# Kernel optimization log

Measured on AMD Instinct MI355X. Metric: run time of the kernel, lower is better.

## Reference

```python
import jax, jax.numpy as jnp
import numpy as np

# Model constants (from init_kwargs)
B, S, D = 2, 2048, 2048          # batch, seq, d_model
E = 64                           # num_routed_experts
TOP_K = 4
BOT = int(D * 0.25)              # bottle_dim = 512
EXP = 1536                       # routed expert hidden (bigmac_expert_size)
DFF = 8192                       # shared expert hidden (d_ff)
Z_LOSS_W = 1e-4
MOE_SCALE = 0.5                  # 1/(1 + [num_shared_experts>0])


def setup_inputs() -> dict:
    key = jax.random.key(0)
    ks = jax.random.split(key, 10)
    std = 0.011
    return {
        "x": jax.random.normal(ks[0], (B, S, D), jnp.float32),
        "router_w": jax.random.normal(ks[1], (E, D), jnp.float32) * 0.02,
        "gate_w": jax.random.normal(ks[2], (DFF, D), jnp.float32) * std,
        "up_w": jax.random.normal(ks[3], (DFF, D), jnp.float32) * std,
        "down_w": jax.random.normal(ks[4], (D, DFF), jnp.float32) * std,
        "w_down": jax.random.normal(ks[5], (BOT, D), jnp.float32) * std,
        "w_up": jax.random.normal(ks[6], (D, BOT), jnp.float32) * std,
        "w12": jax.random.normal(ks[7], (E, BOT, 2 * EXP), jnp.float32) * std,
        "w3": jax.random.normal(ks[8], (E, EXP, BOT), jnp.float32) * std,
    }


def reference(x, router_w, gate_w, up_w, down_w, w_down, w_up, w12, w3):
    b, s, d = x.shape
    h = x.reshape(-1, d)                       # [N, D]
    N = h.shape[0]
    NT = N * TOP_K                             # total routed token-slots

    # ---- router (fp32) ----
    logits = h @ router_w.T                    # [N, E]
    scores = jax.nn.sigmoid(logits)
    z_loss = jnp.mean(jnp.nan_to_num(logits) ** 2) * Z_LOSS_W
    # expert_bias is None -> selection_scores == scores
    _, topk_idx = jax.lax.top_k(scores, TOP_K)             # [N, K]
    topk_logits = jnp.take_along_axis(logits, topk_idx, axis=1)
    gating = jax.nn.softmax(topk_logits, axis=-1)          # [N, K]

    # ---- shared expert (SwiGLU) ----
    shared = (jax.nn.silu(h @ gate_w.T) * (h @ up_w.T)) @ down_w.T  # [N, D]

    # ---- bottleneck down-projection ----
    down = h @ w_down.T                        # [N, BOT]

    # ---- dispatch: sort tokens by expert, capacity-limited padding ----
    flat = topk_idx.reshape(-1)                # [NT]
    order = jnp.argsort(flat)                  # stable sort
    sorted_e = flat[order]
    counts = jax.ops.segment_sum(jnp.ones(NT, jnp.int32), flat, num_segments=E)
    ptr = jnp.cumsum(counts) - counts          # expert start offsets
    local = jnp.arange(NT) - ptr[sorted_e]     # rank within expert
    max_load = (NT // E // 8 + 6) * 8          # capacity per expert
    num_slots = E * max_load
    mask = local < max_load
    slots = sorted_e * max_load + local
    token_idx = jnp.repeat(jnp.arange(N), TOP_K)

    # reverse_map[slot] = source token row (N = dummy row); extra slot absorbs dropped tokens
    rev = jnp.full(num_slots + 1, N, dtype=jnp.int32)
    rev = rev.at[jnp.where(mask, slots, num_slots)].set(token_idx[order].astype(jnp.int32))
    rev = rev[:num_slots]

    h_dummy = jnp.concatenate([down, jnp.zeros((1, BOT), down.dtype)], axis=0)
    padding = h_dummy[rev].reshape(E, max_load, BOT)

    # ---- grouped expert GEMMs ----
    h12 = jnp.einsum('eld,edf->elf', padding, w12)   # [E, max_load, 2*EXP]
    h1, h2 = jnp.split(h12, 2, axis=-1)
    po = jnp.einsum('elf,efd->eld', jax.nn.silu(h1) * h2, w3)  # [E, max_load, BOT]
    po = jnp.concatenate([po.reshape(-1, BOT), jnp.zeros((1, BOT), po.dtype)], axis=0)

    # ---- combine: gather back, weight by gating ----
    gm = jnp.full(NT, num_slots, dtype=jnp.int32)
    gm = gm.at[order].set(jnp.where(mask, slots, num_slots).astype(jnp.int32))
    gathered = po[gm].reshape(N, TOP_K, BOT)
    routed = jnp.einsum('nk,nkd->nd', gating, gathered) @ w_up.T  # [N, D]

    # eval mode: route_scale = 1.0, aux_loss = 0
    out = ((shared + routed) * MOE_SCALE).reshape(b, s, d)
    return out, z_loss
```

## Files before the change

kernel.cpp:

```cpp
#include <hip/hip_runtime.h>

#define DEV __device__ __forceinline__

typedef __attribute__((ext_vector_type(4))) float f4;
typedef __attribute__((ext_vector_type(8))) __bf16 bfrag;
typedef __attribute__((ext_vector_type(4))) unsigned short us4;
typedef __attribute__((ext_vector_type(8))) unsigned short us8;

#define NTOK   4096
#define DMODEL 2048
#define NEXP   64
#define MAXLD  304
#define NSLOT  19456

DEV unsigned short f2bf(float f){
  union { float f; unsigned int i; } u; u.f = f;
  unsigned int r = u.i + 0x7fffu + ((u.i >> 16) & 1u);
  return (unsigned short)(r >> 16);
}
DEV float bf2f(unsigned short b){
  union { unsigned int i; float f; } u; u.i = ((unsigned int)b) << 16;
  return u.f;
}
DEV float silu_f(float g){ return g / (1.0f + __expf(-g)); }

DEV void gl_lds16(const unsigned short* g, unsigned short* l){
  __builtin_amdgcn_global_load_lds(
      (const __attribute__((address_space(1))) void*)g,
      (__attribute__((address_space(3))) void*)l, 16, 0, 0);
}

template<int BM, int EPI>
__global__ __launch_bounds__(512, 1) void gemm2(
    const unsigned short* __restrict__ A, const unsigned short* __restrict__ B,
    void* __restrict__ Cp, const float* __restrict__ addin, int M, int N, int K,
    void* __restrict__ Cp2, void* __restrict__ Cp3)
{
  constexpr int ALD = BM / 128;
  constexpr int MQ  = BM / 64;
  constexpr int HR  = BM / 2;
  __shared__ unsigned short As[2][2][HR * 64];
  __shared__ unsigned short Bs[2][2][128 * 64];

  const int nwg = gridDim.x * gridDim.y;
  int bid = blockIdx.y * gridDim.x + blockIdx.x;
  bid = (bid & 7) * (nwg >> 3) + (bid >> 3);
  const int bx = bid % gridDim.x, by = bid / gridDim.x;
  const int bm = by * BM, bn = bx * 256;

  const int t = threadIdx.x, lane = t & 63, wave = t >> 6;
  const int ha = wave >> 2;
  const int wn = (wave & 3) * 64;
  const int hb = wn >> 7;
  const int cb = wn & 127;
  const int fr = lane & 15, kg = lane >> 4;

  const int r0 = t >> 3;
  const int s0 = (t & 7) ^ (r0 & 7);

#define STG_AH(d_, h_, s_) do {                                                          \
    gl_lds16(A + (long long)(bm + (h_) * HR + r0) * K + (long long)(s_) * 64 + s0 * 8,   \
             &As[d_][h_][(wave * 64) * 8]);                                              \
    if (ALD == 2)                                                                        \
      gl_lds16(A + (long long)(bm + (h_) * HR + r0 + 64) * K + (long long)(s_) * 64 + s0 * 8, \
               &As[d_][h_][(512 + wave * 64) * 8]);                                      \
  } while (0)
#define STG_BH(d_, h_, s_) do {                                                          \
    gl_lds16(B + (long long)(bn + (h_) * 128 + r0) * K + (long long)(s_) * 64 + s0 * 8,  \
             &Bs[d_][h_][(wave * 64) * 8]);                                              \
    gl_lds16(B + (long long)(bn + (h_) * 128 + r0 + 64) * K + (long long)(s_) * 64 + s0 * 8, \
             &Bs[d_][h_][(512 + wave * 64) * 8]);                                        \
  } while (0)

  f4 acc[2 * MQ][4];
#pragma unroll
  for (int m = 0; m < 2 * MQ; ++m)
#pragma unroll
    for (int n = 0; n < 4; ++n) acc[m][n] = f4{0.f, 0.f, 0.f, 0.f};

  const int ns = K >> 6;

  STG_BH(0, 0, 0); STG_AH(0, 0, 0); STG_BH(0, 1, 0); STG_AH(0, 1, 0);
  STG_BH(1, 0, 1); STG_AH(1, 0, 1);
  asm volatile("s_waitcnt vmcnt(%0)" :: "i"(2 + ALD) : "memory");
  __builtin_amdgcn_s_barrier();

  for (int tt = 0; tt < ns; ++tt){
    const int d = tt & 1, nd = d ^ 1;
    bfrag af[MQ][2], bf[2][2][2];

#pragma unroll
    for (int ni = 0; ni < 2; ++ni)
#pragma unroll
      for (int kh = 0; kh < 2; ++kh){
        const int cn = cb + ni * 16 + fr;
        bf[0][ni][kh] = *(const bfrag*)&Bs[d][hb][cn * 64 + ((((kh << 2) | kg) ^ (cn & 7)) << 3)];
      }
#pragma unroll
    for (int mi = 0; mi < MQ; ++mi)
#pragma unroll
      for (int kh = 0; kh < 2; ++kh){
        const int rh = mi * 16 + fr;
        af[mi][kh] = *(const bfrag*)&As[d][ha][rh * 64 + ((((kh << 2) | kg) ^ (rh & 7)) << 3)];
      }
    if (tt + 1 < ns) STG_BH(nd, 1, tt + 1);
    if constexpr (BM == 256) asm volatile("s_waitcnt lgkmcnt(8)");
    else                     asm volatile("s_waitcnt lgkmcnt(4)");
    __builtin_amdgcn_s_barrier();
    asm volatile("s_waitcnt lgkmcnt(0)");
    __builtin_amdgcn_s_setprio(1);
#pragma unroll
    for (int mi = 0; mi < MQ; ++mi)
#pragma unroll
      for (int ni = 0; ni < 2; ++ni)
#pragma unroll
        for (int kh = 0; kh < 2; ++kh)
          acc[mi][ni] = __builtin_amdgcn_mfma_f32_16x16x32_bf16(af[mi][kh], bf[0][ni][kh], acc[mi][ni], 0, 0, 0);
    __builtin_amdgcn_s_setprio(0);
    __builtin_amdgcn_s_barrier();

#pragma unroll
    for (int ni = 0; ni < 2; ++ni)
#pragma unroll
      for (int kh = 0; kh < 2; ++kh){
        const int cn = cb + 32 + ni * 16 + fr;
        bf[1][ni][kh] = *(const bfrag*)&Bs[d][hb][cn * 64 + ((((kh << 2) | kg) ^ (cn & 7)) << 3)];
      }
    if (tt + 1 < ns) STG_AH(nd, 1, tt + 1);
    __builtin_amdgcn_s_barrier();
    asm volatile("s_waitcnt lgkmcnt(0)");
    __builtin_amdgcn_s_setprio(1);
#pragma unroll
    for (int mi = 0; mi < MQ; ++mi)
#pragma unroll
      for (int ni = 0; ni < 2; ++ni)
#pragma unroll
        for (int kh = 0; kh < 2; ++kh)
          acc[mi][2 + ni] = __builtin_amdgcn_mfma_f32_16x16x32_bf16(af[mi][kh], bf[1][ni][kh], acc[mi][2 + ni], 0, 0, 0);
    __builtin_amdgcn_s_setprio(0);
    __builtin_amdgcn_s_barrier();

#pragma unroll
    for (int mi = 0; mi < MQ; ++mi)
#pragma unroll
      for (int kh = 0; kh < 2; ++kh){
        const int rh = MQ * 16 + mi * 16 + fr;
        af[mi][kh] = *(const bfrag*)&As[d][ha][rh * 64 + ((((kh << 2) | kg) ^ (rh & 7)) << 3)];
      }
    if (tt + 2 < ns) STG_BH(d, 0, tt + 2);
    __builtin_amdgcn_s_barrier();
    asm volatile("s_waitcnt lgkmcnt(0)");
    __builtin_amdgcn_s_setprio(1);
#pragma unroll
    for (int mi = 0; mi < MQ; ++mi)
#pragma unroll
      for (int ni = 0; ni < 2; ++ni)
#pragma unroll
        for (int kh = 0; kh < 2; ++kh)
          acc[MQ + mi][2 + ni] = __builtin_amdgcn_mfma_f32_16x16x32_bf16(af[mi][kh], bf[1][ni][kh], acc[MQ + mi][2 + ni], 0, 0, 0);
    __builtin_amdgcn_s_setprio(0);
    __builtin_amdgcn_s_barrier();

    if (tt + 2 < ns) STG_AH(d, 0, tt + 2);
    __builtin_amdgcn_s_barrier();
    __builtin_amdgcn_s_setprio(1);
#pragma unroll
    for (int mi = 0; mi < MQ; ++mi)
#pragma unroll
      for (int ni = 0; ni < 2; ++ni)
#pragma unroll
        for (int kh = 0; kh < 2; ++kh)
          acc[MQ + mi][ni] = __builtin_amdgcn_mfma_f32_16x16x32_bf16(af[mi][kh], bf[0][ni][kh], acc[MQ + mi][ni], 0, 0, 0);
    __builtin_amdgcn_s_setprio(0);
    if (tt + 2 < ns)      asm volatile("s_waitcnt vmcnt(%0)" :: "i"(2 + ALD) : "memory");
    else if (tt + 1 < ns) asm volatile("s_waitcnt vmcnt(0)" ::: "memory");
    if (tt + 1 < ns) __builtin_amdgcn_s_barrier();
  }

  if constexpr (EPI == 3){
    const int base = bn + wn;
    if (base < 16384){
      const int colb = base >> 1;
#pragma unroll
      for (int mh = 0; mh < 2; ++mh)
#pragma unroll
        for (int mi = 0; mi < MQ; ++mi){
          const int row0 = bm + ha * HR + mh * (HR / 2) + mi * 16 + kg * 4;
#pragma unroll
          for (int p = 0; p < 2; ++p){
            f4 g = acc[mh * MQ + mi][2 * p];
            f4 u = acc[mh * MQ + mi][2 * p + 1];
#pragma unroll
            for (int r = 0; r < 4; ++r)
              ((unsigned short*)Cp)[(long long)(row0 + r) * 8192 + colb + p * 16 + fr]
                = f2bf(silu_f(g[r]) * u[r]);
          }
        }
    } else if (base < 16896){
      const int cb2 = base - 16384;
#pragma unroll
      for (int mh = 0; mh < 2; ++mh)
#pragma unroll
        for (int mi = 0; mi < MQ; ++mi){
          const int row0 = bm + ha * HR + mh * (HR / 2) + mi * 16 + kg * 4;
#pragma unroll
          for (int nf = 0; nf < 4; ++nf){
            f4 v = acc[mh * MQ + mi][nf];
#pragma unroll
            for (int r = 0; r < 4; ++r)
              ((unsigned short*)Cp2)[(long long)(row0 + r) * 512 + cb2 + nf * 16 + fr] = f2bf(v[r]);
          }
        }
    } else {
      const int cb3 = base - 16896;
#pragma unroll
      for (int mh = 0; mh < 2; ++mh)
#pragma unroll
        for (int mi = 0; mi < MQ; ++mi){
          const int row0 = bm + ha * HR + mh * (HR / 2) + mi * 16 + kg * 4;
#pragma unroll
          for (int nf = 0; nf < 4; ++nf){
            const int col = cb3 + nf * 16 + fr;
            f4 v = acc[mh * MQ + mi][nf];
            if (col < 64){
#pragma unroll
              for (int r = 0; r < 4; ++r)
                ((float*)Cp3)[(long long)(row0 + r) * 64 + col] = v[r];
            }
          }
        }
    }
    return;
  }
#pragma unroll
  for (int mh = 0; mh < 2; ++mh)
#pragma unroll
    for (int mi = 0; mi < MQ; ++mi){
      const int row0 = bm + ha * HR + mh * (HR / 2) + mi * 16 + kg * 4;
#pragma unroll
      for (int nf = 0; nf < 4; ++nf){
        const int col = bn + wn + nf * 16 + fr;
        f4 v = acc[mh * MQ + mi][nf];
#pragma unroll
        for (int r = 0; r < 4; ++r){
          const long long off = (long long)(row0 + r) * N + col;
          if (EPI == 0)      ((unsigned short*)Cp)[off] = f2bf(v[r]);
          else if (EPI == 1) ((float*)Cp)[off] = v[r];
          else               ((float*)Cp)[off] = (v[r] + addin[off]) * 0.5f;
        }
      }
    }
#undef STG_AH
#undef STG_BH
}

template<int EPI>
__global__ __launch_bounds__(256) void gemm_bt(
    const unsigned short* __restrict__ A, const unsigned short* __restrict__ B,
    void* __restrict__ Cp, const float* __restrict__ addin,
    int M, int N, int K, long long sA, long long sB, long long sC)
{
  __shared__ unsigned short As[128*32];
  __shared__ unsigned short Bs[128*32];
  A += (long long)blockIdx.z * sA;
  B += (long long)blockIdx.z * sB;
  const long long cbase = (long long)blockIdx.z * sC;
  const int bm = blockIdx.y * 128, bn = blockIdx.x * 128;
  const int t = threadIdx.x, wave = t >> 6, lane = t & 63;
  const int wm = (wave >> 1) * 64, wn = (wave & 1) * 64;
  const int fr = lane & 15, kg = lane >> 4;

  f4 acc[4][4];
#pragma unroll
  for (int m = 0; m < 4; ++m)
#pragma unroll
    for (int n = 0; n < 4; ++n)
      acc[m][n] = f4{0.f, 0.f, 0.f, 0.f};

  const int i0 = t, i1 = 256 + t;
  int ar0 = bm + (i0 >> 2); if (ar0 > M - 1) ar0 = M - 1;
  int ar1 = bm + (i1 >> 2); if (ar1 > M - 1) ar1 = M - 1;
  int br0 = bn + (i0 >> 2); if (br0 > N - 1) br0 = N - 1;
  int br1 = bn + (i1 >> 2); if (br1 > N - 1) br1 = N - 1;
  const unsigned short* ap0 = A + (long long)ar0 * K + (i0 & 3) * 8;
  const unsigned short* ap1 = A + (long long)ar1 * K + (i1 & 3) * 8;
  const unsigned short* bp0 = B + (long long)br0 * K + (i0 & 3) * 8;
  const unsigned short* bp1 = B + (long long)br1 * K + (i1 & 3) * 8;
  unsigned short* da0 = As + wave * 512;
  unsigned short* da1 = As + 2048 + wave * 512;
  unsigned short* db0 = Bs + wave * 512;
  unsigned short* db1 = Bs + 2048 + wave * 512;

  for (int k0 = 0; k0 < K; k0 += 32){
    gl_lds16(ap0, da0);
    gl_lds16(ap1, da1);
    gl_lds16(bp0, db0);
    gl_lds16(bp1, db1);
    ap0 += 32; ap1 += 32; bp0 += 32; bp1 += 32;
    __syncthreads();
    bfrag af[4], bfv[4];
#pragma unroll
    for (int m = 0; m < 4; ++m) af[m] = *(const bfrag*)&As[(wm + m*16 + fr)*32 + kg*8];
#pragma unroll
    for (int n = 0; n < 4; ++n) bfv[n] = *(const bfrag*)&Bs[(wn + n*16 + fr)*32 + kg*8];
#pragma unroll
    for (int m = 0; m < 4; ++m)
#pragma unroll
      for (int n = 0; n < 4; ++n)
        acc[m][n] = __builtin_amdgcn_mfma_f32_16x16x32_bf16(af[m], bfv[n], acc[m][n], 0, 0, 0);
    __syncthreads();
  }

  if constexpr (EPI == 3){
    const int colb = (bn + wn) >> 1;
    const int ldo = N >> 1;
#pragma unroll
    for (int m = 0; m < 4; ++m){
      const int row0 = bm + wm + m*16 + kg*4;
#pragma unroll
      for (int p = 0; p < 2; ++p){
        f4 g = acc[m][2*p], u = acc[m][2*p+1];
#pragma unroll
        for (int r = 0; r < 4; ++r){
          const int row = row0 + r;
          if (row < M)
            ((unsigned short*)Cp)[cbase + (long long)row * ldo + colb + p*16 + fr]
              = f2bf(silu_f(g[r]) * u[r]);
        }
      }
    }
    return;
  }
#pragma unroll
  for (int m = 0; m < 4; ++m){
    const int row0 = bm + wm + m*16 + kg*4;
#pragma unroll
    for (int n = 0; n < 4; ++n){
      const int col = bn + wn + n*16 + fr;
      if (col < N){
        f4 v = acc[m][n];
#pragma unroll
        for (int r = 0; r < 4; ++r){
          const int row = row0 + r;
          if (row < M){
            const long long off = cbase + (long long)row * N + col;
            ((unsigned short*)Cp)[off] = f2bf(v[r]);
          }
        }
      }
    }
  }
}

__global__ void cvt_bf16(const float* __restrict__ in, unsigned short* __restrict__ out,
                         long long n4)
{
  long long i = (long long)blockIdx.x * 256 + threadIdx.x;
  if (i >= n4) return;
  float4 v = ((const float4*)in)[i];
  us4 o; o[0] = f2bf(v.x); o[1] = f2bf(v.y); o[2] = f2bf(v.z); o[3] = f2bf(v.w);
  ((us4*)out)[i] = o;
}

__global__ void cvt_rowmap(const float* __restrict__ in, unsigned short* __restrict__ out,
                           int hi)
{
  const long long idx = (long long)blockIdx.x * 256 + threadIdx.x;
  const int row = (int)(idx >> 9);
  const int c4 = ((int)idx & 511) << 2;
  const int orow = ((row >> 4) << 5) | (hi << 4) | (row & 15);
  float4 v = *(const float4*)(in + (long long)row * 2048 + c4);
  us4 o; o[0] = f2bf(v.x); o[1] = f2bf(v.y); o[2] = f2bf(v.z); o[3] = f2bf(v.w);
  *(us4*)(out + (long long)orow * 2048 + c4) = o;
}

template<int MODE>
__global__ __launch_bounds__(256) void transpose_cvt(const float* __restrict__ in,
    unsigned short* __restrict__ out, int R, int C)
{
  __shared__ float tile[32][33];
  const long long z = blockIdx.z;
  const float* ip = in + z * (long long)R * C;
  unsigned short* op = out + z * (long long)R * C;
  const int r0 = blockIdx.y * 32, c0 = blockIdx.x * 32;
  const int t = threadIdx.x;
  const int lr = t >> 3, lc = (t & 7) * 4;
  float4 v = *(const float4*)(ip + (long long)(r0 + lr) * C + c0 + lc);
  tile[lr][lc+0] = v.x; tile[lr][lc+1] = v.y; tile[lr][lc+2] = v.z; tile[lr][lc+3] = v.w;
  __syncthreads();
  const int oc = t >> 3, orr = (t & 7) * 4;
  us4 o;
  o[0] = f2bf(tile[orr+0][oc]); o[1] = f2bf(tile[orr+1][oc]);
  o[2] = f2bf(tile[orr+2][oc]); o[3] = f2bf(tile[orr+3][oc]);
  int c = c0 + oc;
  int orow;
  if (MODE == 1)
    orow = (c < 1536) ? (((c >> 4) << 5) | (c & 15))
                      : ((((c - 1536) >> 4) << 5) | 16 | ((c - 1536) & 15));
  else
    orow = c;
  *(us4*)(op + (long long)orow * R + r0 + orr) = o;
}

__global__ void router_topk(const float* __restrict__ logits, int* __restrict__ topk,
                            float* __restrict__ gating, float* __restrict__ zout)
{
  const int t = threadIdx.x, w = t >> 6, lane = t & 63;
  const int n = blockIdx.x * 4 + w;
  const float lg = logits[(long long)n * 64 + lane];
  float z = lg * lg;
#pragma unroll
  for (int off = 32; off; off >>= 1) z += __shfl_xor(z, off);
  __shared__ float zs[4];
  if (lane == 0) zs[w] = z;
  __syncthreads();
  if (t == 0) atomicAdd(zout, (zs[0]+zs[1]+zs[2]+zs[3]) * (0.0001f / 262144.0f));

  float cur = lg;
  float tl[4]; int ti[4];
#pragma unroll
  for (int k = 0; k < 4; ++k){
    float s = cur; int si = lane;
#pragma unroll
    for (int off = 32; off; off >>= 1){
      float so = __shfl_xor(s, off); int io = __shfl_xor(si, off);
      if (so > s || (so == s && io < si)){ s = so; si = io; }
    }
    tl[k] = s; ti[k] = si;
    if (lane == si) cur = -3.0e38f;
  }
  if (lane == 0){
    const float m0 = tl[0];
    const float e0 = __expf(tl[0]-m0), e1 = __expf(tl[1]-m0),
                e2 = __expf(tl[2]-m0), e3 = __expf(tl[3]-m0);
    const float inv = 1.0f / (e0 + e1 + e2 + e3);
    topk[n*4+0] = ti[0]; topk[n*4+1] = ti[1]; topk[n*4+2] = ti[2]; topk[n*4+3] = ti[3];
    gating[n*4+0] = e0*inv; gating[n*4+1] = e1*inv; gating[n*4+2] = e2*inv; gating[n*4+3] = e3*inv;
  }
}

__global__ void scan_route(const int* __restrict__ topk, int* __restrict__ gm,
                           int* __restrict__ rev, int* __restrict__ counts)
{
  const int e = blockIdx.x;
  const int t = threadIdx.x, w = t >> 6, lane = t & 63;
  __shared__ int wtot[4];
  int running = 0;
  for (int c = 0; c < 16384; c += 256){
    const int j = c + t;
    const bool p = (topk[j] == e);
    const unsigned long long m = __ballot(p);
    const int prefix = __popcll(m & ((1ull << lane) - 1ull));
    if (lane == 0) wtot[w] = __popcll(m);
    __syncthreads();
    int woff = 0;
#pragma unroll
    for (int i = 0; i < 4; ++i){ if (i < w) woff += wtot[i]; }
    const int btot = wtot[0] + wtot[1] + wtot[2] + wtot[3];
    if (p){
      const int rank = running + woff + prefix;
      gm[j] = (rank < MAXLD) ? (e * MAXLD + rank) : NSLOT;
      if (rank < MAXLD) rev[e * MAXLD + rank] = j >> 2;
    }
    running += btot;
    __syncthreads();
  }
  if (t == 0) counts[e] = running;
}

__global__ void gather_pad(const unsigned short* __restrict__ down, const int* __restrict__ rev,
                           const int* __restrict__ counts, unsigned short* __restrict__ pad)
{
  const int idx = blockIdx.x * 256 + threadIdx.x;
  const int s = idx >> 6, c8 = (idx & 63) * 8;
  const int e = s / MAXLD;
  const int r = s - e * MAXLD;
  int cnt = counts[e]; if (cnt > MAXLD) cnt = MAXLD;
  us8 v = {0,0,0,0,0,0,0,0};
  if (r < cnt){
    const int tok = rev[s];
    v = *(const us8*)(down + (long long)tok * 512 + c8);
  }
  *(us8*)(pad + (long long)s * 512 + c8) = v;
}

__global__ void combine_moe(const unsigned short* __restrict__ po, const int* __restrict__ gm,
                            const float* __restrict__ gating, unsigned short* __restrict__ routed)
{
  const int idx = blockIdx.x * 256 + threadIdx.x;
  const int n = idx >> 6, c8 = (idx & 63) * 8;
  float acc[8] = {0,0,0,0,0,0,0,0};
#pragma unroll
  for (int k = 0; k < 4; ++k){
    const int slot = gm[n*4 + k];
    if (slot < NSLOT){
      const float gw = gating[n*4 + k];
      us8 v = *(const us8*)(po + (long long)slot * 512 + c8);
#pragma unroll
      for (int j = 0; j < 8; ++j) acc[j] += gw * bf2f(v[j]);
    }
  }
  us8 o;
#pragma unroll
  for (int j = 0; j < 8; ++j) o[j] = f2bf(acc[j]);
  *(us8*)(routed + (long long)n * 512 + c8) = o;
}

extern "C" void kernel_launch(void* const* d_in, const int* in_sizes, int n_in,
                              void* d_out, int out_size, void* d_ws, size_t ws_size,
                              hipStream_t stream)
{
  const float* x      = (const float*)d_in[0];
  const float* rw     = (const float*)d_in[1];
  const float* gate_w = (const float*)d_in[2];
  const float* up_w   = (const float*)d_in[3];
  const float* down_w = (const float*)d_in[4];
  const float* w_down = (const float*)d_in[5];
  const float* w_up   = (const float*)d_in[6];
  const float* w12    = (const float*)d_in[7];
  const float* w3     = (const float*)d_in[8];
  float* out = (float*)d_out;

  char* ws = (char*)d_ws;
  unsigned short* HBF   = (unsigned short*)(ws + 0ull);
  unsigned short* BBIG  = (unsigned short*)(ws + 16777216ull);
  unsigned short* DWB   = (unsigned short*)(ws + 87031808ull);
  unsigned short* WUB   = (unsigned short*)(ws + 120586240ull);
  unsigned short* W12I  = (unsigned short*)(ws + 122683392ull);
  unsigned short* W3T   = (unsigned short*)(ws + 324009984ull);
  float*          LOGIT = (float*)(ws + 424673280ull);
  int*            TOPKI = (int*)(ws + 425721856ull);
  float*          GATE4 = (float*)(ws + 425787392ull);
  int*            GM    = (int*)(ws + 425852928ull);
  int*            CNT   = (int*)(ws + 425918464ull);
  int*            REV   = (int*)(ws + 425919488ull);
  unsigned short* ACTS  = (unsigned short*)(ws + 426000384ull);
  unsigned short* AEXP  = (unsigned short*)(ws + 493109248ull);
  float*          SHRD  = (float*)(ws + 552878080ull);
  unsigned short* DNB   = (unsigned short*)(ws + 586432512ull);
  unsigned short* PAD   = (unsigned short*)(ws + 590626816ull);
  unsigned short* PO    = (unsigned short*)(ws + 610549760ull);
  unsigned short* RTD   = (unsigned short*)(ws + 630472704ull);

  hipMemsetAsync((char*)d_out + 8388608ull * 4, 0, 4, stream);
  hipMemsetAsync(BBIG + 16960ull * 2048, 0, 192ull * 2048 * 2, stream);

  cvt_bf16<<<8192,  256, 0, stream>>>(x, HBF, 2097152);
  cvt_rowmap<<<16384, 256, 0, stream>>>(gate_w, BBIG, 0);
  cvt_rowmap<<<16384, 256, 0, stream>>>(up_w,   BBIG, 1);
  cvt_bf16<<<1024,  256, 0, stream>>>(w_down, BBIG + 16384ull * 2048, 262144);
  cvt_bf16<<<128,   256, 0, stream>>>(rw,     BBIG + 16896ull * 2048, 32768);
  cvt_bf16<<<16384, 256, 0, stream>>>(down_w, DWB, 4194304);
  cvt_bf16<<<1024,  256, 0, stream>>>(w_up,   WUB, 262144);
  transpose_cvt<1><<<dim3(96,16,64), 256, 0, stream>>>(w12, W12I, 512, 3072);
  transpose_cvt<0><<<dim3(16,48,64), 256, 0, stream>>>(w3,  W3T,  1536, 512);

  gemm2<256,3><<<dim3(67,16), 512, 0, stream>>>(HBF, BBIG, ACTS, nullptr,
                                                4096, 17152, 2048, DNB, LOGIT);

  router_topk<<<1024, 256, 0, stream>>>(LOGIT, TOPKI, GATE4, out + 8388608);
  scan_route<<<64, 256, 0, stream>>>(TOPKI, GM, REV, CNT);
  gather_pad<<<4864, 256, 0, stream>>>(DNB, REV, CNT, PAD);

  gemm_bt<3><<<dim3(24,3,64), 256, 0, stream>>>(PAD, W12I, AEXP, nullptr,
                                                304, 3072, 512, 155648, 1572864, 466944);
  gemm_bt<0><<<dim3(4,3,64), 256, 0, stream>>>(AEXP, W3T, PO, nullptr,
                                               304, 512, 1536, 466944, 786432, 155648);
  combine_moe<<<1024, 256, 0, stream>>>(PO, GM, GATE4, RTD);

  gemm2<128,1><<<dim3(8,32), 512, 0, stream>>>(ACTS, DWB, SHRD, nullptr,
                                               4096, 2048, 8192, nullptr, nullptr);
  gemm2<128,2><<<dim3(8,32), 512, 0, stream>>>(RTD, WUB, out, SHRD,
                                               4096, 2048, 512, nullptr, nullptr);
}
```

Before: 1.124 ms.

## Use pipelined gemm2 for expert GEMMs and split-K the shared down projection

Generalizes gemm2 with batch strides, separate leading dimensions and row clamping, so the grouped expert GEMMs (SwiGLU epilogue and plain) run on the double-buffered 512-thread kernel instead of the simple gemm_bt. The shared-expert down projection is split along K into two batched halves with a 256-row tile, producing two fp32 partials. The final w_up GEMM sums both partials in its epilogue. This trades extra fp32 partial traffic and padded-row waste on 304-row experts for better pipelining and more workgroups on the 8192-deep GEMM.

```diff
diff --git a/kernel.cpp b/kernel.cpp
--- a/kernel.cpp
+++ b/kernel.cpp
@@ -33,7 +33,9 @@
 template<int BM, int EPI>
 __global__ __launch_bounds__(512, 1) void gemm2(
     const unsigned short* __restrict__ A, const unsigned short* __restrict__ B,
-    void* __restrict__ Cp, const float* __restrict__ addin, int M, int N, int K,
+    void* __restrict__ Cp, const float* __restrict__ add0, const float* __restrict__ add1,
+    int M, int N, int K, int lda, int ldb,
+    long long sA, long long sB, long long sC,
     void* __restrict__ Cp2, void* __restrict__ Cp3)
 {
   constexpr int ALD = BM / 128;
@@ -42,9 +44,13 @@
   __shared__ unsigned short As[2][2][HR * 64];
   __shared__ unsigned short Bs[2][2][128 * 64];
 
+  A += (long long)blockIdx.z * sA;
+  B += (long long)blockIdx.z * sB;
+  const long long cbase = (long long)blockIdx.z * sC;
+
   const int nwg = gridDim.x * gridDim.y;
   int bid = blockIdx.y * gridDim.x + blockIdx.x;
-  bid = (bid & 7) * (nwg >> 3) + (bid >> 3);
+  if ((nwg & 7) == 0) bid = (bid & 7) * (nwg >> 3) + (bid >> 3);
   const int bx = bid % gridDim.x, by = bid / gridDim.x;
   const int bm = by * BM, bn = bx * 256;
 
@@ -59,16 +65,19 @@
   const int s0 = (t & 7) ^ (r0 & 7);
 
 #define STG_AH(d_, h_, s_) do {                                                          \
-    gl_lds16(A + (long long)(bm + (h_) * HR + r0) * K + (long long)(s_) * 64 + s0 * 8,   \
+    int rA0 = bm + (h_) * HR + r0; if (rA0 > M - 1) rA0 = M - 1;                         \
+    gl_lds16(A + (long long)rA0 * lda + (long long)(s_) * 64 + s0 * 8,                   \
              &As[d_][h_][(wave * 64) * 8]);                                              \
-    if (ALD == 2)                                                                        \
-      gl_lds16(A + (long long)(bm + (h_) * HR + r0 + 64) * K + (long long)(s_) * 64 + s0 * 8, \
+    if (ALD == 2){                                                                       \
+      int rA1 = bm + (h_) * HR + r0 + 64; if (rA1 > M - 1) rA1 = M - 1;                  \
+      gl_lds16(A + (long long)rA1 * lda + (long long)(s_) * 64 + s0 * 8,                 \
                &As[d_][h_][(512 + wave * 64) * 8]);                                      \
+    }                                                                                    \
   } while (0)
 #define STG_BH(d_, h_, s_) do {                                                          \
-    gl_lds16(B + (long long)(bn + (h_) * 128 + r0) * K + (long long)(s_) * 64 + s0 * 8,  \
+    gl_lds16(B + (long long)(bn + (h_) * 128 + r0) * ldb + (long long)(s_) * 64 + s0 * 8,\
              &Bs[d_][h_][(wave * 64) * 8]);                                              \
-    gl_lds16(B + (long long)(bn + (h_) * 128 + r0 + 64) * K + (long long)(s_) * 64 + s0 * 8, \
+    gl_lds16(B + (long long)(bn + (h_) * 128 + r0 + 64) * ldb + (long long)(s_) * 64 + s0 * 8, \
              &Bs[d_][h_][(512 + wave * 64) * 8]);                                        \
   } while (0)
 
@@ -232,6 +241,29 @@
     }
     return;
   }
+  if constexpr (EPI == 4){
+    const int colb = (bn + wn) >> 1;
+    const int ldo = N >> 1;
+#pragma unroll
+    for (int mh = 0; mh < 2; ++mh)
+#pragma unroll
+      for (int mi = 0; mi < MQ; ++mi){
+        const int row0 = bm + ha * HR + mh * (HR / 2) + mi * 16 + kg * 4;
+#pragma unroll
+        for (int p = 0; p < 2; ++p){
+          f4 g = acc[mh * MQ + mi][2 * p];
+          f4 u = acc[mh * MQ + mi][2 * p + 1];
+#pragma unroll
+          for (int r = 0; r < 4; ++r){
+            const int row = row0 + r;
+            if (row < M)
+              ((unsigned short*)Cp)[cbase + (long long)row * ldo + colb + p * 16 + fr]
+                = f2bf(silu_f(g[r]) * u[r]);
+          }
+        }
+      }
+    return;
+  }
 #pragma unroll
   for (int mh = 0; mh < 2; ++mh)
 #pragma unroll
@@ -243,113 +275,18 @@
         f4 v = acc[mh * MQ + mi][nf];
 #pragma unroll
         for (int r = 0; r < 4; ++r){
-          const long long off = (long long)(row0 + r) * N + col;
-          if (EPI == 0)      ((unsigned short*)Cp)[off] = f2bf(v[r]);
-          else if (EPI == 1) ((float*)Cp)[off] = v[r];
-          else               ((float*)Cp)[off] = (v[r] + addin[off]) * 0.5f;
+          const int row = row0 + r;
+          if (row < M){
+            const long long off = cbase + (long long)row * N + col;
+            if (EPI == 0)      ((unsigned short*)Cp)[off] = f2bf(v[r]);
+            else if (EPI == 1) ((float*)Cp)[off] = v[r];
+            else               ((float*)Cp)[off] = (v[r] + add0[off] + add1[off]) * 0.5f;
+          }
         }
       }
     }
 #undef STG_AH
 #undef STG_BH
-}
-
-template<int EPI>
-__global__ __launch_bounds__(256) void gemm_bt(
-    const unsigned short* __restrict__ A, const unsigned short* __restrict__ B,
-    void* __restrict__ Cp, const float* __restrict__ addin,
-    int M, int N, int K, long long sA, long long sB, long long sC)
-{
-  __shared__ unsigned short As[128*32];
-  __shared__ unsigned short Bs[128*32];
-  A += (long long)blockIdx.z * sA;
-  B += (long long)blockIdx.z * sB;
-  const long long cbase = (long long)blockIdx.z * sC;
-  const int bm = blockIdx.y * 128, bn = blockIdx.x * 128;
-  const int t = threadIdx.x, wave = t >> 6, lane = t & 63;
-  const int wm = (wave >> 1) * 64, wn = (wave & 1) * 64;
-  const int fr = lane & 15, kg = lane >> 4;
-
-  f4 acc[4][4];
-#pragma unroll
-  for (int m = 0; m < 4; ++m)
-#pragma unroll
-    for (int n = 0; n < 4; ++n)
-      acc[m][n] = f4{0.f, 0.f, 0.f, 0.f};
-
-  const int i0 = t, i1 = 256 + t;
-  int ar0 = bm + (i0 >> 2); if (ar0 > M - 1) ar0 = M - 1;
-  int ar1 = bm + (i1 >> 2); if (ar1 > M - 1) ar1 = M - 1;
-  int br0 = bn + (i0 >> 2); if (br0 > N - 1) br0 = N - 1;
-  int br1 = bn + (i1 >> 2); if (br1 > N - 1) br1 = N - 1;
-  const unsigned short* ap0 = A + (long long)ar0 * K + (i0 & 3) * 8;
-  const unsigned short* ap1 = A + (long long)ar1 * K + (i1 & 3) * 8;
-  const unsigned short* bp0 = B + (long long)br0 * K + (i0 & 3) * 8;
-  const unsigned short* bp1 = B + (long long)br1 * K + (i1 & 3) * 8;
-  unsigned short* da0 = As + wave * 512;
-  unsigned short* da1 = As + 2048 + wave * 512;
-  unsigned short* db0 = Bs + wave * 512;
-  unsigned short* db1 = Bs + 2048 + wave * 512;
-
-  for (int k0 = 0; k0 < K; k0 += 32){
-    gl_lds16(ap0, da0);
-    gl_lds16(ap1, da1);
-    gl_lds16(bp0, db0);
-    gl_lds16(bp1, db1);
-    ap0 += 32; ap1 += 32; bp0 += 32; bp1 += 32;
-    __syncthreads();
-    bfrag af[4], bfv[4];
-#pragma unroll
-    for (int m = 0; m < 4; ++m) af[m] = *(const bfrag*)&As[(wm + m*16 + fr)*32 + kg*8];
-#pragma unroll
-    for (int n = 0; n < 4; ++n) bfv[n] = *(const bfrag*)&Bs[(wn + n*16 + fr)*32 + kg*8];
-#pragma unroll
-    for (int m = 0; m < 4; ++m)
-#pragma unroll
-      for (int n = 0; n < 4; ++n)
-        acc[m][n] = __builtin_amdgcn_mfma_f32_16x16x32_bf16(af[m], bfv[n], acc[m][n], 0, 0, 0);
-    __syncthreads();
-  }
-
-  if constexpr (EPI == 3){
-    const int colb = (bn + wn) >> 1;
-    const int ldo = N >> 1;
-#pragma unroll
-    for (int m = 0; m < 4; ++m){
-      const int row0 = bm + wm + m*16 + kg*4;
-#pragma unroll
-      for (int p = 0; p < 2; ++p){
-        f4 g = acc[m][2*p], u = acc[m][2*p+1];
-#pragma unroll
-        for (int r = 0; r < 4; ++r){
-          const int row = row0 + r;
-          if (row < M)
-            ((unsigned short*)Cp)[cbase + (long long)row * ldo + colb + p*16 + fr]
-              = f2bf(silu_f(g[r]) * u[r]);
-        }
-      }
-    }
-    return;
-  }
-#pragma unroll
-  for (int m = 0; m < 4; ++m){
-    const int row0 = bm + wm + m*16 + kg*4;
-#pragma unroll
-    for (int n = 0; n < 4; ++n){
-      const int col = bn + wn + n*16 + fr;
-      if (col < N){
-        f4 v = acc[m][n];
-#pragma unroll
-        for (int r = 0; r < 4; ++r){
-          const int row = row0 + r;
-          if (row < M){
-            const long long off = cbase + (long long)row * N + col;
-            ((unsigned short*)Cp)[off] = f2bf(v[r]);
-          }
-        }
-      }
-    }
-  }
 }
 
 __global__ void cvt_bf16(const float* __restrict__ in, unsigned short* __restrict__ out,
@@ -537,10 +474,10 @@
   unsigned short* ACTS  = (unsigned short*)(ws + 426000384ull);
   unsigned short* AEXP  = (unsigned short*)(ws + 493109248ull);
   float*          SHRD  = (float*)(ws + 552878080ull);
-  unsigned short* DNB   = (unsigned short*)(ws + 586432512ull);
-  unsigned short* PAD   = (unsigned short*)(ws + 590626816ull);
-  unsigned short* PO    = (unsigned short*)(ws + 610549760ull);
-  unsigned short* RTD   = (unsigned short*)(ws + 630472704ull);
+  unsigned short* DNB   = (unsigned short*)(ws + 619987072ull);
+  unsigned short* PAD   = (unsigned short*)(ws + 624181376ull);
+  unsigned short* PO    = (unsigned short*)(ws + 644104192ull);
+  unsigned short* RTD   = (unsigned short*)(ws + 664027136ull);
 
   hipMemsetAsync((char*)d_out + 8388608ull * 4, 0, 4, stream);
   hipMemsetAsync(BBIG + 16960ull * 2048, 0, 192ull * 2048 * 2, stream);
@@ -555,21 +492,23 @@
   transpose_cvt<1><<<dim3(96,16,64), 256, 0, stream>>>(w12, W12I, 512, 3072);
   transpose_cvt<0><<<dim3(16,48,64), 256, 0, stream>>>(w3,  W3T,  1536, 512);
 
-  gemm2<256,3><<<dim3(67,16), 512, 0, stream>>>(HBF, BBIG, ACTS, nullptr,
-                                                4096, 17152, 2048, DNB, LOGIT);
+  gemm2<256,3><<<dim3(67,16,1), 512, 0, stream>>>(HBF, BBIG, ACTS, nullptr, nullptr,
+      4096, 17152, 2048, 2048, 2048, 0, 0, 0, DNB, LOGIT);
 
   router_topk<<<1024, 256, 0, stream>>>(LOGIT, TOPKI, GATE4, out + 8388608);
   scan_route<<<64, 256, 0, stream>>>(TOPKI, GM, REV, CNT);
+
+  gemm2<256,1><<<dim3(8,16,2), 512, 0, stream>>>(ACTS, DWB, SHRD, nullptr, nullptr,
+      4096, 2048, 4096, 8192, 8192, 4096LL, 4096LL, 8388608LL, nullptr, nullptr);
+
   gather_pad<<<4864, 256, 0, stream>>>(DNB, REV, CNT, PAD);
 
-  gemm_bt<3><<<dim3(24,3,64), 256, 0, stream>>>(PAD, W12I, AEXP, nullptr,
-                                                304, 3072, 512, 155648, 1572864, 466944);
-  gemm_bt<0><<<dim3(4,3,64), 256, 0, stream>>>(AEXP, W3T, PO, nullptr,
-                                               304, 512, 1536, 466944, 786432, 155648);
+  gemm2<128,4><<<dim3(12,3,64), 512, 0, stream>>>(PAD, W12I, AEXP, nullptr, nullptr,
+      304, 3072, 512, 512, 512, 155648LL, 1572864LL, 466944LL, nullptr, nullptr);
+  gemm2<128,0><<<dim3(2,3,64), 512, 0, stream>>>(AEXP, W3T, PO, nullptr, nullptr,
+      304, 512, 1536, 1536, 1536, 466944LL, 786432LL, 155648LL, nullptr, nullptr);
   combine_moe<<<1024, 256, 0, stream>>>(PO, GM, GATE4, RTD);
 
-  gemm2<128,1><<<dim3(8,32), 512, 0, stream>>>(ACTS, DWB, SHRD, nullptr,
-                                               4096, 2048, 8192, nullptr, nullptr);
-  gemm2<128,2><<<dim3(8,32), 512, 0, stream>>>(RTD, WUB, out, SHRD,
-                                               4096, 2048, 512, nullptr, nullptr);
-}
+  gemm2<128,2><<<dim3(8,32,1), 512, 0, stream>>>(RTD, WUB, out, SHRD, SHRD + 8388608,
+      4096, 2048, 512, 512, 512, 0, 0, 0, nullptr, nullptr);
+}
```

After: 1.116 ms, median of 2. About the same (-0.7%).
